# Optimization experiments

Hardware: AMD Instinct MI355X
Metric: run time of the kernel (lower is better)

## Reference

```python
import jax, jax.numpy as jnp
import numpy as np

B, L, D, H, I = 4, 1024, 2048, 16, 8192
DH = D // H  # 128
EPS = 1e-6


def setup_inputs() -> dict:
    key = jax.random.key(0)
    ks = jax.random.split(key, 10)
    hidden_states = jax.random.normal(ks[0], (B, L, D), dtype=jnp.float32)
    # additive causal mask [B,1,L,L]: 0 on allowed, large negative on masked
    causal = jnp.tril(jnp.ones((L, L), dtype=bool))
    attention_mask = jnp.where(causal, 0.0, -1e9).astype(jnp.float32)
    attention_mask = jnp.broadcast_to(attention_mask[None, None], (B, 1, L, L))
    # RoPE tables [B,L,DH]
    inv_freq = 1.0 / (10000.0 ** (jnp.arange(0, DH, 2, dtype=jnp.float32) / DH))
    pos = jnp.arange(L, dtype=jnp.float32)
    freqs = pos[:, None] * inv_freq[None, :]            # [L, DH/2]
    emb = jnp.concatenate([freqs, freqs], axis=-1)       # [L, DH]
    cos = jnp.broadcast_to(jnp.cos(emb)[None], (B, L, DH)).astype(jnp.float32)
    sin = jnp.broadcast_to(jnp.sin(emb)[None], (B, L, DH)).astype(jnp.float32)
    s = 0.02
    return {
        "hidden_states": hidden_states,
        "attention_mask": attention_mask,
        "cos": cos,
        "sin": sin,
        "q_w": jax.random.normal(ks[1], (D, D), jnp.float32) * s,
        "k_w": jax.random.normal(ks[2], (D, D), jnp.float32) * s,
        "v_w": jax.random.normal(ks[3], (D, D), jnp.float32) * s,
        "o_w": jax.random.normal(ks[4], (D, D), jnp.float32) * s,
        "gate_w": jax.random.normal(ks[5], (I, D), jnp.float32) * s,
        "up_w": jax.random.normal(ks[6], (I, D), jnp.float32) * s,
        "down_w": jax.random.normal(ks[7], (D, I), jnp.float32) * s,
        "ln1_w": jnp.ones((D,), jnp.float32),
        "ln2_w": jnp.ones((D,), jnp.float32),
    }


def _rms_norm(x, w):
    var = jnp.mean(jnp.square(x), axis=-1, keepdims=True)
    return x * jax.lax.rsqrt(var + EPS) * w


def _rotate_half(x):
    x1, x2 = jnp.split(x, 2, axis=-1)
    return jnp.concatenate([-x2, x1], axis=-1)


def reference(hidden_states, attention_mask, cos, sin, q_w, k_w, v_w, o_w,
              gate_w, up_w, down_w, ln1_w, ln2_w):
    residual = hidden_states
    h = _rms_norm(hidden_states, ln1_w)                       # [B,L,D]
    # QKV projections (torch Linear: x @ W^T)
    def heads(x, w):
        return (x @ w.T).reshape(B, L, H, DH).transpose(0, 2, 1, 3)  # [B,H,L,DH]
    q, k, v = heads(h, q_w), heads(h, k_w), heads(h, v_w)
    cos_b, sin_b = cos[:, None], sin[:, None]                 # [B,1,L,DH]
    q = q * cos_b + _rotate_half(q) * sin_b
    k = k * cos_b + _rotate_half(k) * sin_b
    scores = jnp.einsum('bhqd,bhkd->bhqk', q, k) / jnp.sqrt(jnp.float32(DH))
    scores = scores + attention_mask                          # [B,H,L,L]
    attn = jax.nn.softmax(scores, axis=-1)
    ctx = jnp.einsum('bhqk,bhkd->bhqd', attn, v)              # [B,H,L,DH]
    ctx = ctx.transpose(0, 2, 1, 3).reshape(B, L, D)
    attn_out = ctx @ o_w.T
    h1 = residual + attn_out
    h2 = _rms_norm(h1, ln2_w)
    mlp = (jax.nn.silu(h2 @ gate_w.T) * (h2 @ up_w.T)) @ down_w.T
    out = h1 + mlp
    return out, attn
```

## Files before the change

kernel.cpp:

```cpp
#include <hip/hip_runtime.h>


typedef __bf16 bf16;
typedef __bf16 bf16x8 __attribute__((ext_vector_type(8)));
typedef __bf16 bf16x4 __attribute__((ext_vector_type(4)));
typedef float  f32x4  __attribute__((ext_vector_type(4)));

constexpr int   kB  = 4;
constexpr int   kL  = 1024;
constexpr int   kD  = 2048;
constexpr int   kH  = 16;
constexpr int   kI  = 8192;
constexpr int   kDH = 128;
constexpr int   kQKV = 3 * kD;
constexpr float kEps = 1e-6f;
constexpr float kScoreScale = 0.08838834764831845f;

typedef __attribute__((address_space(1))) void gvoid_t;
typedef __attribute__((address_space(3))) void lvoid_t;

__device__ __forceinline__ void gload_lds16(const void* g, void* l) {
  __builtin_amdgcn_global_load_lds((gvoid_t*)g, (lvoid_t*)l, 16, 0, 0);
}

__global__ __launch_bounds__(256) void cast_f32_bf16_kernel(
    const float* __restrict__ x, bf16* __restrict__ y, long n) {
  long i = ((long)blockIdx.x * 256 + threadIdx.x) * 4;
  long stride = (long)gridDim.x * 256 * 4;
  for (; i < n; i += stride) {
    const float4 v = *reinterpret_cast<const float4*>(x + i);
    bf16x4 o;
    o[0] = (bf16)v.x; o[1] = (bf16)v.y; o[2] = (bf16)v.z; o[3] = (bf16)v.w;
    *reinterpret_cast<bf16x4*>(y + i) = o;
  }
}

__global__ __launch_bounds__(256) void add_inplace_kernel(
    float* __restrict__ o, const float* __restrict__ p, long n) {
  long i = ((long)blockIdx.x * 256 + threadIdx.x) * 4;
  const long stride = (long)gridDim.x * 1024;
  for (; i < n; i += stride) {
    float4 a = *(float4*)(o + i);
    const float4 b = *(const float4*)(p + i);
    a.x += b.x; a.y += b.y; a.z += b.z; a.w += b.w;
    *(float4*)(o + i) = a;
  }
}

__global__ __launch_bounds__(256) void rmsnorm_kernel(
    const float* __restrict__ x, const float* __restrict__ w,
    bf16* __restrict__ out) {
  const long row = blockIdx.x;
  const float* xr = x + row * (long)kD;
  bf16* orow = out + row * (long)kD;
  const int t = threadIdx.x;

  float4 v0 = *(const float4*)(xr + t * 8);
  float4 v1 = *(const float4*)(xr + t * 8 + 4);
  float ss = v0.x * v0.x + v0.y * v0.y + v0.z * v0.z + v0.w * v0.w +
             v1.x * v1.x + v1.y * v1.y + v1.z * v1.z + v1.w * v1.w;

  __shared__ float red[4];
  for (int off = 32; off > 0; off >>= 1) ss += __shfl_down(ss, off);
  if ((t & 63) == 0) red[t >> 6] = ss;
  __syncthreads();
  const float tot = red[0] + red[1] + red[2] + red[3];
  const float rs = rsqrtf(tot / (float)kD + kEps);

  float4 w0 = *(const float4*)(w + t * 8);
  float4 w1 = *(const float4*)(w + t * 8 + 4);
  bf16x8 o;
  o[0] = (bf16)(v0.x * rs * w0.x); o[1] = (bf16)(v0.y * rs * w0.y);
  o[2] = (bf16)(v0.z * rs * w0.z); o[3] = (bf16)(v0.w * rs * w0.w);
  o[4] = (bf16)(v1.x * rs * w1.x); o[5] = (bf16)(v1.y * rs * w1.y);
  o[6] = (bf16)(v1.z * rs * w1.z); o[7] = (bf16)(v1.w * rs * w1.w);
  *(bf16x8*)(orow + t * 8) = o;
}

__global__ __launch_bounds__(256) void rope_kernel(
    bf16* __restrict__ qkv, const float* __restrict__ cosb,
    const float* __restrict__ sinb) {
  const long row = blockIdx.x;
  const float* cr = cosb + row * (long)kDH;
  const float* sr = sinb + row * (long)kDH;
  bf16* qr = qkv + row * (long)kQKV;
  bf16* kr = qr + kD;
  const int t = threadIdx.x;
#pragma unroll
  for (int it = 0; it < 4; ++it) {
    const int p = it * 256 + t;
    const int h = p >> 6, i = p & 63;
    const int i0 = h * kDH + i, i1 = i0 + 64;
    const float c0 = cr[i], s0 = sr[i], c1 = cr[i + 64], s1 = sr[i + 64];
    const float q0 = (float)qr[i0], q1 = (float)qr[i1];
    qr[i0] = (bf16)(q0 * c0 - q1 * s0);
    qr[i1] = (bf16)(q1 * c1 + q0 * s1);
    const float k0 = (float)kr[i0], k1 = (float)kr[i1];
    kr[i0] = (bf16)(k0 * c0 - k1 * s0);
    kr[i1] = (bf16)(k1 * c1 + k0 * s1);
  }
}

__global__ __launch_bounds__(256) void transpose_v_kernel(
    const bf16* __restrict__ qkv, bf16* __restrict__ vT) {
  __shared__ bf16 tile[32][33];
  const int z = blockIdx.z, b = z / kH, h = z % kH;
  const bf16* src = qkv + (long)b * kL * kQKV + 2 * kD + h * kDH;
  bf16* dst = vT + (long)z * kDH * kL;
  const int l0 = blockIdx.x * 32, d0 = blockIdx.y * 32;
  const int tx = threadIdx.x & 31, ty = threadIdx.x >> 5;
  for (int r = ty; r < 32; r += 8)
    tile[r][tx] = src[(long)(l0 + r) * kQKV + d0 + tx];
  __syncthreads();
  for (int r = ty; r < 32; r += 8)
    dst[(long)(d0 + r) * kL + l0 + tx] = tile[tx][r];
}

__global__ __launch_bounds__(256) void merge_stats_kernel(
    const float2* __restrict__ sp, float2* __restrict__ sm) {
  const int idx = blockIdx.x * 256 + threadIdx.x;
  const int row = idx & 1023;
  const int n = ((row >> 7) + 1) * 2;
  const float2* p = sp + ((long)idx << 4);
  float M = -3.0e38f;
  for (int i = 0; i < n; ++i) M = fmaxf(M, p[i].x);
  float S = 0.f;
  for (int i = 0; i < n; ++i) S += p[i].y * expf(p[i].x - M);
  sm[idx] = make_float2(M, 1.0f / S);
}

enum { EPI_NONE = 0, EPI_ADD = 1, EPI_SILU = 3, EPI_SPLIT = 5,
       EPI_PASS1 = 6, EPI_PASS2 = 7 };

template <typename OutT, int EPI, bool AF32, int NF, bool CK>
__device__ __forceinline__ void gemm_body(
    const void* __restrict__ Ap, long sAo, long sAi, int lda,
    const bf16* __restrict__ Bp, long sBo, long sBi, int ldb,
    OutT* Cp, long sCo, long sCi, int ldc,
    const void* Ep, long sEo, long sEi, int lde,
    float scale, int Hdiv, int M, int N, int K) {
  constexpr int BN = 32 * NF;
  constexpr int ACH = 512;
  constexpr int BCH = BN * 4;
  static_assert((EPI != EPI_PASS1 && EPI != EPI_PASS2) || NF == 4, "pass NF=4");

  const int z = blockIdx.z;
  const int zo = z / Hdiv, zi = z % Hdiv;

  const bf16* A = nullptr;
  const float* Af = nullptr;
  if constexpr (AF32) Af = (const float*)Ap + zo * sAo + zi * sAi;
  else                A  = (const bf16*)Ap + zo * sAo + zi * sAi;
  const bf16* Bw = Bp + zo * sBo + zi * sBi;
  OutT* C = Cp + zo * sCo + zi * sCi;

  const int t = threadIdx.x;
  const int m0 = blockIdx.y * 128, n0 = blockIdx.x * BN;

  if constexpr (EPI == EPI_PASS1) {
    if (blockIdx.x > blockIdx.y) return;
  }
  if constexpr (EPI == EPI_PASS2) {
    if (blockIdx.x > blockIdx.y) {
      for (int e = t; e < 128 * 32; e += 256) {
        const int row = e >> 5, col = (e & 31) * 4;
        *(float4*)&C[(long)(m0 + row) * ldc + n0 + col] =
            make_float4(0.f, 0.f, 0.f, 0.f);
      }
      return;
    }
  }

  __shared__ __align__(16) bf16 lsA[2][128 * 32];
  __shared__ __align__(16) bf16 lsB[2][BN * 32];

  const int wave = t >> 6, lane = t & 63;
  const int wm = (wave >> 1) * 64, wn = (wave & 1) * (NF * 16);
  const int lr = lane & 15, lg = lane >> 4;

  f32x4 acc[4][NF] = {};

  auto stage = [&](int buf, int k0) {
    if constexpr (AF32) {
#pragma unroll
      for (int c = 0; c < 2; ++c) {
        const int id = c * 256 + t;
        const int row = id >> 2, col = (id & 3) * 8;
        const float* src = Af + (long)(m0 + row) * lda + k0 + col;
        const float4 u0 = *(const float4*)src;
        const float4 u1 = *(const float4*)(src + 4);
        bf16x8 wv;
        wv[0] = (bf16)u0.x; wv[1] = (bf16)u0.y; wv[2] = (bf16)u0.z; wv[3] = (bf16)u0.w;
        wv[4] = (bf16)u1.x; wv[5] = (bf16)u1.y; wv[6] = (bf16)u1.z; wv[7] = (bf16)u1.w;
        *(bf16x8*)&lsA[buf][id * 8] = wv;
        if (NF == 4 || c == 0)
          gload_lds16(Bw + (long)(n0 + row) * ldb + k0 + col, &lsB[buf][id * 8]);
      }
    } else {
#pragma unroll
      for (int c = 0; c < (ACH + BCH) / 256; ++c) {
        const int id = c * 256 + t;
        if (id < ACH) {
          const int row = id >> 2, col = (id & 3) * 8;
          gload_lds16(A + (long)(m0 + row) * lda + k0 + col, &lsA[buf][id * 8]);
        } else {
          const int fid = id - ACH;
          const int row = fid >> 2, col = (fid & 3) * 8;
          gload_lds16(Bw + (long)(n0 + row) * ldb + k0 + col, &lsB[buf][fid * 8]);
        }
      }
    }
  };

  auto compute = [&](int buf) {
    bf16x8 af[4], bfr[NF];
#pragma unroll
    for (int i = 0; i < 4; ++i)
      af[i] = *(const bf16x8*)&lsA[buf][(wm + i * 16 + lr) * 32 + lg * 8];
#pragma unroll
    for (int j = 0; j < NF; ++j)
      bfr[j] = *(const bf16x8*)&lsB[buf][(wn + j * 16 + lr) * 32 + lg * 8];
#pragma unroll
    for (int i = 0; i < 4; ++i)
#pragma unroll
      for (int j = 0; j < NF; ++j)
        acc[i][j] = __builtin_amdgcn_mfma_f32_16x16x32_bf16(af[i], bfr[j],
                                                            acc[i][j], 0, 0, 0);
  };

  const int Klim = CK ? (m0 + 128) : K;

  stage(0, 0);
  __syncthreads();
  int cur = 0;
  for (int k0 = 0; k0 < Klim - 32; k0 += 32) {
    stage(cur ^ 1, k0 + 32);
    compute(cur);
    __syncthreads();
    cur ^= 1;
  }
  compute(cur);

  if constexpr (EPI == EPI_PASS1) {
    float2* statsP = (float2*)Ep;
    const int half = wn >> 6, nt = blockIdx.x;
#pragma unroll
    for (int i = 0; i < 4; ++i) {
#pragma unroll
      for (int r = 0; r < 4; ++r) {
        const int rowg = m0 + wm + i * 16 + lg * 4 + r;
        float v[NF];
        float mx = -3.0e38f;
#pragma unroll
        for (int j = 0; j < NF; ++j) {
          const int colg = n0 + wn + j * 16 + lr;
          v[j] = acc[i][j][r] * scale + (colg > rowg ? -1.0e9f : 0.0f);
          mx = fmaxf(mx, v[j]);
        }
        for (int sh = 1; sh <= 8; sh <<= 1) mx = fmaxf(mx, __shfl_xor(mx, sh));
        float s = 0.f;
#pragma unroll
        for (int j = 0; j < NF; ++j) s += expf(v[j] - mx);
        for (int sh = 1; sh <= 8; sh <<= 1) s += __shfl_xor(s, sh);
        if (lr == 0)
          statsP[(((long)(z << 10) + rowg) << 4) + nt * 2 + half] =
              make_float2(mx, s);
      }
    }
  } else if constexpr (EPI == EPI_PASS2) {
    const float2* sm = (const float2*)Ep;
#pragma unroll
    for (int i = 0; i < 4; ++i) {
#pragma unroll
      for (int j = 0; j < NF; ++j) {
        const int colg = n0 + wn + j * 16 + lr;
#pragma unroll
        for (int r = 0; r < 4; ++r) {
          const int rowg = m0 + wm + i * 16 + lg * 4 + r;
          float p = 0.0f;
          if (colg <= rowg) {
            const float2 st = sm[(z << 10) + rowg];
            p = expf(acc[i][j][r] * scale - st.x) * st.y;
          }
          C[(long)rowg * ldc + colg] = (OutT)p;
        }
      }
    }
  } else {
    const float* Ef = (const float*)Ep;
    const bf16* Eb = (const bf16*)Ep;
    long ebase = 0;
    if constexpr (EPI == EPI_ADD || EPI == EPI_SILU)
      ebase = zo * sEo + zi * sEi;
#pragma unroll
    for (int i = 0; i < 4; ++i) {
#pragma unroll
      for (int j = 0; j < NF; ++j) {
        const int col = n0 + wn + j * 16 + lr;
#pragma unroll
        for (int r = 0; r < 4; ++r) {
          const int rowi = m0 + wm + i * 16 + lg * 4 + r;
          float val = acc[i][j][r] * scale;
          const long idx = (long)rowi * ldc + col;
          if constexpr (EPI == EPI_SPLIT) {
            if (zo == 0) C[idx] = val + C[idx];
            else         ((float*)Ep)[idx] = val;
          } else {
            if constexpr (EPI == EPI_ADD)
              val += Ef[ebase + (long)rowi * lde + col];
            if constexpr (EPI == EPI_SILU) {
              const float g = (float)Eb[ebase + (long)rowi * lde + col];
              val = (g / (1.0f + expf(-g))) * val;
            }
            C[idx] = (OutT)val;
          }
        }
      }
    }
  }
}

#define GEMM_ARGS                                                        \
  const void* __restrict__ Ap, long sAo, long sAi, int lda,              \
  const bf16* __restrict__ Bp, long sBo, long sBi, int ldb,              \
  void* Cp, long sCo, long sCi, int ldc,                                 \
  const void* Ep, long sEo, long sEi, int lde,                           \
  float scale, int Hdiv, int M, int N, int K
#define GEMM_PASS Ap, sAo, sAi, lda, Bp, sBo, sBi, ldb, (OUT_T*)Cp, sCo, \
  sCi, ldc, Ep, sEo, sEi, lde, scale, Hdiv, M, N, K

#define DEF_GEMM(NAME, OUT_TY, EPI_V, AF32_V, NF_V, CK_V)                \
  __global__ __launch_bounds__(256) void NAME(GEMM_ARGS) {               \
    using OUT_T = OUT_TY;                                                \
    gemm_body<OUT_T, EPI_V, AF32_V, NF_V, CK_V>(GEMM_PASS);              \
  }

DEF_GEMM(gemm_qkv,   bf16,  EPI_NONE,  false, 4, false)
DEF_GEMM(gemm_sc1,   float, EPI_PASS1, false, 4, false)
DEF_GEMM(gemm_sc2,   float, EPI_PASS2, false, 4, false)
DEF_GEMM(gemm_ctx,   bf16,  EPI_NONE,  true,  2, true)
DEF_GEMM(gemm_oproj, float, EPI_ADD,   false, 2, false)
DEF_GEMM(gemm_gate,  bf16,  EPI_NONE,  false, 4, false)
DEF_GEMM(gemm_up,    bf16,  EPI_SILU,  false, 4, false)
DEF_GEMM(gemm_downs, float, EPI_SPLIT, false, 2, false)

extern "C" void kernel_launch(void* const* d_in, const int* in_sizes, int n_in,
                              void* d_out, int out_size, void* d_ws,
                              size_t ws_size, hipStream_t stream) {
  (void)in_sizes; (void)n_in; (void)out_size; (void)ws_size;

  const float* hidden = (const float*)d_in[0];
  const float* cosb   = (const float*)d_in[2];
  const float* sinb   = (const float*)d_in[3];
  const float* q_w    = (const float*)d_in[4];
  const float* k_w    = (const float*)d_in[5];
  const float* v_w    = (const float*)d_in[6];
  const float* o_w    = (const float*)d_in[7];
  const float* gate_w = (const float*)d_in[8];
  const float* up_w   = (const float*)d_in[9];
  const float* down_w = (const float*)d_in[10];
  const float* ln1    = (const float*)d_in[11];
  const float* ln2    = (const float*)d_in[12];

  float* out  = (float*)d_out;
  float* attn = out + (long)kB * kL * kD;

  bf16* wsb = (bf16*)d_ws;
  long off = 0;
  bf16* WQKV = wsb + off; off += 3L * kD * kD;
  bf16* WO   = wsb + off; off += (long)kD * kD;
  bf16* WBIG = wsb + off; off += (long)kI * kD;
  bf16* HBF  = wsb + off; off += (long)kB * kL * kD;
  bf16* QKV  = wsb + off; off += (long)kB * kL * kQKV;
  bf16* GBUF = wsb + off; off += (long)kB * kL * kI;

  float2* STATS_P = (float2*)HBF;
  float2* STATS_M = STATS_P + (64L * 1024 * 16);
  float* DPART = (float*)(QKV + (long)kB * kL * kD);

  const long DD = (long)kD * kD;
  const long ID = (long)kI * kD;
  const int  ML = kB * kL;

  cast_f32_bf16_kernel<<<dim3((int)(DD / 1024)), 256, 0, stream>>>(q_w, WQKV, DD);
  cast_f32_bf16_kernel<<<dim3((int)(DD / 1024)), 256, 0, stream>>>(k_w, WQKV + DD, DD);
  cast_f32_bf16_kernel<<<dim3((int)(DD / 1024)), 256, 0, stream>>>(v_w, WQKV + 2 * DD, DD);
  cast_f32_bf16_kernel<<<dim3((int)(DD / 1024)), 256, 0, stream>>>(o_w, WO, DD);

  rmsnorm_kernel<<<ML, 256, 0, stream>>>(hidden, ln1, HBF);

  gemm_qkv<<<dim3(kQKV / 128, ML / 128, 1), 256, 0, stream>>>(
      HBF, 0, 0, kD, WQKV, 0, 0, kD, QKV, 0, 0, kQKV,
      nullptr, 0, 0, 0, 1.0f, 1, ML, kQKV, kD);

  rope_kernel<<<ML, 256, 0, stream>>>(QKV, cosb, sinb);

  transpose_v_kernel<<<dim3(kL / 32, kDH / 32, kB * kH), 256, 0, stream>>>(QKV, GBUF);

  gemm_sc1<<<dim3(kL / 128, kL / 128, kB * kH), 256, 0, stream>>>(
      QKV, (long)kL * kQKV, kDH, kQKV,
      QKV + kD, (long)kL * kQKV, kDH, kQKV,
      attn, (long)kH * kL * kL, (long)kL * kL, kL,
      STATS_P, 0, 0, 0,
      kScoreScale, kH, kL, kL, kDH);

  merge_stats_kernel<<<256, 256, 0, stream>>>(STATS_P, STATS_M);

  gemm_sc2<<<dim3(kL / 128, kL / 128, kB * kH), 256, 0, stream>>>(
      QKV, (long)kL * kQKV, kDH, kQKV,
      QKV + kD, (long)kL * kQKV, kDH, kQKV,
      attn, (long)kH * kL * kL, (long)kL * kL, kL,
      STATS_M, 0, 0, 0,
      kScoreScale, kH, kL, kL, kDH);

  gemm_ctx<<<dim3(kDH / 64, kL / 128, kB * kH), 256, 0, stream>>>(
      attn, (long)kH * kL * kL, (long)kL * kL, kL,
      GBUF, (long)kH * kDH * kL, (long)kDH * kL, kL,
      HBF, (long)kL * kD, kDH, kD,
      nullptr, 0, 0, 0, 1.0f, kH, kL, kDH, kL);

  gemm_oproj<<<dim3(kD / 64, ML / 128, 1), 256, 0, stream>>>(
      HBF, 0, 0, kD, WO, 0, 0, kD, out, 0, 0, kD,
      hidden, 0, 0, kD, 1.0f, 1, ML, kD, kD);

  bf16* H2 = QKV;
  rmsnorm_kernel<<<ML, 256, 0, stream>>>(out, ln2, H2);

  cast_f32_bf16_kernel<<<dim3((int)(ID / 1024)), 256, 0, stream>>>(gate_w, WBIG, ID);
  gemm_gate<<<dim3(kI / 128, ML / 128, 1), 256, 0, stream>>>(
      H2, 0, 0, kD, WBIG, 0, 0, kD, GBUF, 0, 0, kI,
      nullptr, 0, 0, 0, 1.0f, 1, ML, kI, kD);

  cast_f32_bf16_kernel<<<dim3((int)(ID / 1024)), 256, 0, stream>>>(up_w, WBIG, ID);
  gemm_up<<<dim3(kI / 128, ML / 128, 1), 256, 0, stream>>>(
      H2, 0, 0, kD, WBIG, 0, 0, kD, GBUF, 0, 0, kI,
      GBUF, 0, 0, kI, 1.0f, 1, ML, kI, kD);

  cast_f32_bf16_kernel<<<dim3((int)(ID / 1024)), 256, 0, stream>>>(down_w, WBIG, ID);
  gemm_downs<<<dim3(kD / 64, ML / 128, 2), 256, 0, stream>>>(
      GBUF, 4096, 0, kI, WBIG, 4096, 0, kI, out, 0, 0, kD,
      DPART, 0, 0, kD, 1.0f, 1, ML, kD, kI / 2);

  add_inplace_kernel<<<2048, 256, 0, stream>>>(out, DPART, (long)ML * kD);
}
```

Before: 1.195 ms.

## Use raw barriers with partial vmcnt waits and drop split-K for down projection

For bf16-A GEMMs, the main loop now waits only for the previous stage's async LDS loads using explicit s_waitcnt vmcnt counts plus raw s_barrier, rather than __syncthreads, which drains all outstanding loads. This lets the next tile's global-to-LDS loads stay in flight during compute. Separately, the down projection no longer uses a two-way split-K with a partial buffer and a separate add kernel; it runs a single full-K GEMM that adds into the output in its epilogue. That removes the partial-buffer traffic and one launch, but halves the grid parallelism for that GEMM and relies on the hand-counted vmcnt values being correct.

New measurement: 1.153 ms. -3.5%, faster.

```diff
diff --git a/kernel.cpp b/kernel.cpp
--- a/kernel.cpp
+++ b/kernel.cpp
@@ -23,6 +23,14 @@
   __builtin_amdgcn_global_load_lds((gvoid_t*)g, (lvoid_t*)l, 16, 0, 0);
 }
 
+#define ASM_VMCNT(n) asm volatile("s_waitcnt vmcnt(" #n ")" ::: "memory")
+
+__device__ __forceinline__ void bar_raw() {
+  asm volatile("" ::: "memory");
+  __builtin_amdgcn_s_barrier();
+  asm volatile("" ::: "memory");
+}
+
 __global__ __launch_bounds__(256) void cast_f32_bf16_kernel(
     const float* __restrict__ x, bf16* __restrict__ y, long n) {
   long i = ((long)blockIdx.x * 256 + threadIdx.x) * 4;
@@ -32,18 +40,6 @@
     bf16x4 o;
     o[0] = (bf16)v.x; o[1] = (bf16)v.y; o[2] = (bf16)v.z; o[3] = (bf16)v.w;
     *reinterpret_cast<bf16x4*>(y + i) = o;
-  }
-}
-
-__global__ __launch_bounds__(256) void add_inplace_kernel(
-    float* __restrict__ o, const float* __restrict__ p, long n) {
-  long i = ((long)blockIdx.x * 256 + threadIdx.x) * 4;
-  const long stride = (long)gridDim.x * 1024;
-  for (; i < n; i += stride) {
-    float4 a = *(float4*)(o + i);
-    const float4 b = *(const float4*)(p + i);
-    a.x += b.x; a.y += b.y; a.z += b.z; a.w += b.w;
-    *(float4*)(o + i) = a;
   }
 }
 
@@ -129,7 +125,7 @@
   sm[idx] = make_float2(M, 1.0f / S);
 }
 
-enum { EPI_NONE = 0, EPI_ADD = 1, EPI_SILU = 3, EPI_SPLIT = 5,
+enum { EPI_NONE = 0, EPI_ADD = 1, EPI_SILU = 3, EPI_OUTADD = 4,
        EPI_PASS1 = 6, EPI_PASS2 = 7 };
 
 template <typename OutT, int EPI, bool AF32, int NF, bool CK>
@@ -229,17 +225,32 @@
   };
 
   const int Klim = CK ? (m0 + 128) : K;
-
-  stage(0, 0);
-  __syncthreads();
   int cur = 0;
-  for (int k0 = 0; k0 < Klim - 32; k0 += 32) {
-    stage(cur ^ 1, k0 + 32);
+
+  if constexpr (AF32) {
+    stage(0, 0);
+    __syncthreads();
+    for (int k0 = 0; k0 < Klim - 32; k0 += 32) {
+      stage(cur ^ 1, k0 + 32);
+      compute(cur);
+      __syncthreads();
+      cur ^= 1;
+    }
     compute(cur);
-    __syncthreads();
-    cur ^= 1;
-  }
-  compute(cur);
+  } else {
+    stage(0, 0);
+    for (int k0 = 0; k0 < Klim - 32; k0 += 32) {
+      stage(cur ^ 1, k0 + 32);
+      if constexpr (NF == 4) ASM_VMCNT(4); else ASM_VMCNT(3);
+      bar_raw();
+      compute(cur);
+      bar_raw();
+      cur ^= 1;
+    }
+    ASM_VMCNT(0);
+    bar_raw();
+    compute(cur);
+  }
 
   if constexpr (EPI == EPI_PASS1) {
     float2* statsP = (float2*)Ep;
@@ -302,18 +313,15 @@
           const int rowi = m0 + wm + i * 16 + lg * 4 + r;
           float val = acc[i][j][r] * scale;
           const long idx = (long)rowi * ldc + col;
-          if constexpr (EPI == EPI_SPLIT) {
-            if (zo == 0) C[idx] = val + C[idx];
-            else         ((float*)Ep)[idx] = val;
-          } else {
-            if constexpr (EPI == EPI_ADD)
-              val += Ef[ebase + (long)rowi * lde + col];
-            if constexpr (EPI == EPI_SILU) {
-              const float g = (float)Eb[ebase + (long)rowi * lde + col];
-              val = (g / (1.0f + expf(-g))) * val;
-            }
-            C[idx] = (OutT)val;
+          if constexpr (EPI == EPI_ADD)
+            val += Ef[ebase + (long)rowi * lde + col];
+          if constexpr (EPI == EPI_SILU) {
+            const float g = (float)Eb[ebase + (long)rowi * lde + col];
+            val = (g / (1.0f + expf(-g))) * val;
           }
+          if constexpr (EPI == EPI_OUTADD)
+            val += (float)C[idx];
+          C[idx] = (OutT)val;
         }
       }
     }
@@ -335,14 +343,14 @@
     gemm_body<OUT_T, EPI_V, AF32_V, NF_V, CK_V>(GEMM_PASS);              \
   }
 
-DEF_GEMM(gemm_qkv,   bf16,  EPI_NONE,  false, 4, false)
-DEF_GEMM(gemm_sc1,   float, EPI_PASS1, false, 4, false)
-DEF_GEMM(gemm_sc2,   float, EPI_PASS2, false, 4, false)
-DEF_GEMM(gemm_ctx,   bf16,  EPI_NONE,  true,  2, true)
-DEF_GEMM(gemm_oproj, float, EPI_ADD,   false, 2, false)
-DEF_GEMM(gemm_gate,  bf16,  EPI_NONE,  false, 4, false)
-DEF_GEMM(gemm_up,    bf16,  EPI_SILU,  false, 4, false)
-DEF_GEMM(gemm_downs, float, EPI_SPLIT, false, 2, false)
+DEF_GEMM(gemm_qkv,   bf16,  EPI_NONE,   false, 4, false)
+DEF_GEMM(gemm_sc1,   float, EPI_PASS1,  false, 4, false)
+DEF_GEMM(gemm_sc2,   float, EPI_PASS2,  false, 4, false)
+DEF_GEMM(gemm_ctx,   bf16,  EPI_NONE,   true,  2, true)
+DEF_GEMM(gemm_oproj, float, EPI_ADD,    false, 2, false)
+DEF_GEMM(gemm_gate,  bf16,  EPI_NONE,   false, 4, false)
+DEF_GEMM(gemm_up,    bf16,  EPI_SILU,   false, 4, false)
+DEF_GEMM(gemm_down,  float, EPI_OUTADD, false, 2, false)
 
 extern "C" void kernel_launch(void* const* d_in, const int* in_sizes, int n_in,
                               void* d_out, int out_size, void* d_ws,
@@ -376,7 +384,6 @@
 
   float2* STATS_P = (float2*)HBF;
   float2* STATS_M = STATS_P + (64L * 1024 * 16);
-  float* DPART = (float*)(QKV + (long)kB * kL * kD);
 
   const long DD = (long)kD * kD;
   const long ID = (long)kI * kD;
@@ -437,9 +444,7 @@
       GBUF, 0, 0, kI, 1.0f, 1, ML, kI, kD);
 
   cast_f32_bf16_kernel<<<dim3((int)(ID / 1024)), 256, 0, stream>>>(down_w, WBIG, ID);
-  gemm_downs<<<dim3(kD / 64, ML / 128, 2), 256, 0, stream>>>(
-      GBUF, 4096, 0, kI, WBIG, 4096, 0, kI, out, 0, 0, kD,
-      DPART, 0, 0, kD, 1.0f, 1, ML, kD, kI / 2);
-
-  add_inplace_kernel<<<2048, 256, 0, stream>>>(out, DPART, (long)ML * kD);
-}
+  gemm_down<<<dim3(kD / 64, ML / 128, 1), 256, 0, stream>>>(
+      GBUF, 0, 0, kI, WBIG, 0, 0, kI, out, 0, 0, kD,
+      nullptr, 0, 0, 0, 1.0f, 1, ML, kD, kI);
+}
```
